# Performance work log

Measured on AMD Instinct MI355X. Metric: run time of the kernel, lower is better.

The kernel has to match this reference:

```python
import jax, jax.numpy as jnp
import numpy as np

N_NODES = 10000
N_EDGES = 160000
IN_FEATS = 512
H_FEATS = 512
NUM_CLASSES = 128


def setup_inputs() -> dict:
    key = jax.random.key(0)
    ks = jax.random.split(key, 7)
    h = jax.random.normal(ks[0], (N_NODES, IN_FEATS), dtype=jnp.float32)
    W1 = jax.random.normal(ks[1], (2 * IN_FEATS, H_FEATS), dtype=jnp.float32) * 0.02
    b1 = jax.random.normal(ks[2], (H_FEATS,), dtype=jnp.float32) * 0.02
    W2 = jax.random.normal(ks[3], (2 * H_FEATS, NUM_CLASSES), dtype=jnp.float32) * 0.02
    b2 = jax.random.normal(ks[4], (NUM_CLASSES,), dtype=jnp.float32) * 0.02
    src = jax.random.randint(ks[5], (N_EDGES,), 0, N_NODES, dtype=jnp.int32)
    dst = jax.random.randint(ks[6], (N_EDGES,), 0, N_NODES, dtype=jnp.int32)
    return {"h": h, "W1": W1, "b1": b1, "W2": W2, "b2": b2, "src": src, "dst": dst}


def _weighted_sage_conv(h, W, b, src, dst, n_nodes):
    # message = u_mul_e('h','w') with w == ones -> just gather source features
    msg = h[src]  # [E, d]
    # fn.mean reduce at destination: segment-sum / in-degree (0 if no in-edges)
    s = jax.ops.segment_sum(msg, dst, num_segments=n_nodes)  # [N, d]
    cnt = jax.ops.segment_sum(jnp.ones((src.shape[0],), h.dtype), dst, num_segments=n_nodes)
    h_N = s / jnp.maximum(cnt, 1.0)[:, None]
    h_total = jnp.concatenate([h, h_N], axis=1)  # [N, 2d]
    return h_total @ W + b


def reference(h, W1, b1, W2, b2, src, dst):
    n = h.shape[0]
    h1 = jax.nn.relu(_weighted_sage_conv(h, W1, b1, src, dst, n))
    return _weighted_sage_conv(h1, W2, b2, src, dst, n)
```

## Files before the change

### kernel.cpp

```cpp
#include <hip/hip_runtime.h>

typedef unsigned short u16;
typedef unsigned char u8;
typedef __attribute__((ext_vector_type(2))) float floatx2;
typedef __attribute__((ext_vector_type(4))) float floatx4;
typedef __attribute__((ext_vector_type(8))) __bf16 bf16x8;
typedef __attribute__((ext_vector_type(2))) unsigned short us2;
typedef __attribute__((ext_vector_type(4))) unsigned short us4;
typedef __attribute__((ext_vector_type(8))) unsigned short us8;
typedef __attribute__((ext_vector_type(2))) unsigned int u32x2;

static __device__ __forceinline__ float b2f(u16 v) {
    union { unsigned u; float f; } x; x.u = ((unsigned)v) << 16; return x.f;
}
static __device__ __forceinline__ u16 f2b(float f) {
    union { float f; unsigned u; } x; x.f = f;
    unsigned u = x.u;
    return (u16)((u + 0x7fffu + ((u >> 16) & 1u)) >> 16);
}

#define GLOAD_LDS16(g, l) __builtin_amdgcn_global_load_lds( \
    (const __attribute__((address_space(1))) void*)(g),     \
    (__attribute__((address_space(3))) void*)(l), 16, 0, 0)

#define CAP 64
#define SPILLMAX 4096

static __device__ __forceinline__ int detect_blk(const u16* __restrict__ p,
                                                 int nelem, int* sh) {
    if (threadIdx.x == 0) *sh = 0;
    __syncthreads();
    const int lim = nelem < 512 ? nelem : 512;
    int found = 0;
    for (int j = threadIdx.x; 2 * j < lim; j += 256) {
        unsigned v = p[2 * j] & 0x7fffu;
        if (v >= 0x4280u) found = 1;
    }
    if (found) atomicOr(sh, 1);
    __syncthreads();
    return *sh;
}

static __device__ __forceinline__ int xcd_swz(int L, int nwg) {
    const int q = nwg >> 3, r = nwg & 7;
    const int x = L & 7, i = L >> 3;
    return (x < r ? x * (q + 1) : r * (q + 1) + (x - r) * q) + i;
}

__global__ __launch_bounds__(256) void k_d1(
    const int* __restrict__ src, const int* __restrict__ dst, int E, int Nn,
    int* __restrict__ cnt, int* __restrict__ bucket,
    int* __restrict__ nspill, int* __restrict__ spill,
    const void* __restrict__ h, const void* __restrict__ W1,
    const void* __restrict__ b1, const void* __restrict__ W2,
    const void* __restrict__ b2,
    u16* __restrict__ Hb, u16* __restrict__ W1T, u16* __restrict__ W2T,
    u16* __restrict__ b1c, u16* __restrict__ b2c, int* __restrict__ flags,
    int nFill, int nHb) {
    __shared__ u16 tile[32][33];
    __shared__ int sh;
    const int b = blockIdx.x;
    const int t = threadIdx.x;

    if (b < nFill) {
        int e = b * 256 + t;
        if (e < E) {
            int d = dst[e], s = src[e];
            if ((unsigned)d < (unsigned)Nn && (unsigned)s < (unsigned)Nn) {
                int p = atomicAdd(&cnt[d], 1);
                if (p < CAP) bucket[d * CAP + p] = s;
                else {
                    int q = atomicAdd(nspill, 1);
                    if (q < SPILLMAX) { spill[2 * q] = d; spill[2 * q + 1] = s; }
                }
            }
        }
        return;
    }
    if (b < nFill + nHb) {
        const int f = detect_blk((const u16*)h, Nn * 512, &sh);
        int i = ((b - nFill) * 256 + t) * 8;
        if (i >= Nn * 512) return;
        if (f) {
            const floatx4* s = (const floatx4*)((const float*)h + i);
            floatx4 v0 = s[0], v1 = s[1];
            us8 o;
            o[0] = f2b(v0[0]); o[1] = f2b(v0[1]); o[2] = f2b(v0[2]); o[3] = f2b(v0[3]);
            o[4] = f2b(v1[0]); o[5] = f2b(v1[1]); o[6] = f2b(v1[2]); o[7] = f2b(v1[3]);
            *(us8*)(Hb + i) = o;
        } else {
            *(us8*)(Hb + i) = *(const us8*)((const u16*)h + i);
        }
        return;
    }
    if (b < nFill + nHb + 512) {
        const int f = detect_blk((const u16*)W1, 1024 * 512, &sh);
        int sub = b - nFill - nHb;
        int half = sub >> 8, idx = sub & 255;
        const int bx = (idx & 15) * 32, by = (idx >> 4) * 32;
        const int koff = half * 512, noff = half * 512;
        const int tx = t & 31, ty = t >> 5;
        for (int i = ty; i < 32; i += 8) {
            long id = (long)(koff + by + i) * 512 + (bx + tx);
            tile[i][tx] = f ? f2b(((const float*)W1)[id]) : ((const u16*)W1)[id];
        }
        __syncthreads();
        for (int i = ty; i < 32; i += 8)
            W1T[(long)(noff + bx + i) * 512 + (by + tx)] = tile[tx][i];
        return;
    }
    if (b < nFill + nHb + 640) {
        const int f = detect_blk((const u16*)W2, 1024 * 128, &sh);
        int sub = b - nFill - nHb - 512;
        int half = sub >> 6, idx = sub & 63;
        const int bx = (idx & 3) * 32, by = (idx >> 2) * 32;
        const int koff = half * 512, noff = half * 128;
        const int tx = t & 31, ty = t >> 5;
        for (int i = ty; i < 32; i += 8) {
            long id = (long)(koff + by + i) * 128 + (bx + tx);
            tile[i][tx] = f ? f2b(((const float*)W2)[id]) : ((const u16*)W2)[id];
        }
        __syncthreads();
        for (int i = ty; i < 32; i += 8)
            W2T[(long)(noff + bx + i) * 512 + (by + tx)] = tile[tx][i];
        return;
    }
    {
        const int f1 = detect_blk((const u16*)b1, 512, &sh);
        for (int i = t; i < 512; i += 256)
            b1c[i] = f1 ? f2b(((const float*)b1)[i]) : ((const u16*)b1)[i];
        const int f2 = detect_blk((const u16*)b2, 128, &sh);
        if (t < 128)
            b2c[t] = f2 ? f2b(((const float*)b2)[t]) : ((const u16*)b2)[t];
        const int fh = detect_blk((const u16*)h, Nn * 512, &sh);
        if (t == 0) flags[0] = fh;
    }
}

__device__ __forceinline__ void gemm_acc64(const u16* __restrict__ A,
                                           const u16* __restrict__ Bt,
                                           long brow, int bobs,
                                           floatx4 acc[4][2], u16* lA, u16* lB) {
    const int tid = threadIdx.x;
    const int wv = tid >> 6;
    const int ln = tid & 63;
    const int lrow = ln >> 2;
    const int lk = (ln & 3) * 8;
    const int m0 = ln & 15;
    const int kq = (ln >> 4) * 8;
    const int wc = wv * 32;

#pragma unroll
    for (int i = 0; i < 4; ++i)
#pragma unroll
        for (int j = 0; j < 2; ++j) acc[i][j] = (floatx4){0.f, 0.f, 0.f, 0.f};

    const u16* gA = A + (brow + wv * 16 + lrow) * 512 + lk;

    auto STAGE = [&](int kt, int sel) {
        u16* dA = lA + sel * 2048 + wv * 512;
        u16* dB = lB + sel * 4096;
        GLOAD_LDS16(gA + kt, dA);
#pragma unroll
        for (int ii = 0; ii < 2; ++ii) {
            const int c = ii * 4 + wv;
            GLOAD_LDS16(Bt + (long)(bobs + c * 16 + lrow) * 512 + kt + lk,
                        dB + c * 512);
        }
    };
    auto COMPUTE = [&](int sel) {
        const u16* rA = lA + sel * 2048;
        const u16* rB = lB + sel * 4096;
        bf16x8 af[4], bf[2];
#pragma unroll
        for (int i = 0; i < 4; ++i)
            af[i] = *(const bf16x8*)(rA + (i * 16 + m0) * 32 + kq);
#pragma unroll
        for (int j = 0; j < 2; ++j)
            bf[j] = *(const bf16x8*)(rB + (wc + j * 16 + m0) * 32 + kq);
#pragma unroll
        for (int i = 0; i < 4; ++i)
#pragma unroll
            for (int j = 0; j < 2; ++j)
                acc[i][j] = __builtin_amdgcn_mfma_f32_16x16x32_bf16(af[i], bf[j],
                                                                    acc[i][j], 0, 0, 0);
    };

    STAGE(0, 0);
    for (int t = 0; t < 15; ++t) {
        const int sel = t & 1;
        STAGE((t + 1) << 5, sel ^ 1);
        asm volatile("s_waitcnt vmcnt(3)" ::: "memory");
        __builtin_amdgcn_s_barrier();
        COMPUTE(sel);
        asm volatile("s_waitcnt lgkmcnt(0)" ::: "memory");
        __builtin_amdgcn_s_barrier();
    }
    asm volatile("s_waitcnt vmcnt(0)" ::: "memory");
    __builtin_amdgcn_s_barrier();
    COMPUTE(1);
}

__global__ __launch_bounds__(256) void k_gemm1_64(
    const u16* __restrict__ A, const u16* __restrict__ Bt,
    u16* __restrict__ C1s, u8* __restrict__ P1, int Mstore) {
    __shared__ __align__(16) u16 lA[2 * 64 * 32];
    __shared__ __align__(16) u16 lB[2 * 128 * 32];
    const int L = blockIdx.y * gridDim.x + blockIdx.x;
    const int T = xcd_swz(L, gridDim.x * gridDim.y);
    const int by = T & 7;
    const int bcol = by * 128;
    const long brow = (long)(T >> 3) * 64;
    floatx4 acc[4][2];
    gemm_acc64(A, Bt, brow, bcol, acc, lA, lB);

    const int ln = threadIdx.x & 63;
    const int wv = threadIdx.x >> 6;
    const int wc = wv * 32;
    const int m0 = ln & 15;
    const int q4 = (ln >> 4) * 4;
    if (by < 4) {
#pragma unroll
        for (int i = 0; i < 4; ++i)
#pragma unroll
            for (int r = 0; r < 4; ++r) {
                long row = brow + i * 16 + q4 + r;
                if (row < Mstore) {
#pragma unroll
                    for (int j = 0; j < 2; ++j)
                        C1s[row * 512 + (bcol + wc + j * 16 + m0)] = f2b(acc[i][j][r]);
                }
            }
    } else {
        const int coff = bcol - 512;
#pragma unroll
        for (int i = 0; i < 4; ++i)
#pragma unroll
            for (int r = 0; r < 4; ++r) {
                long row = brow + i * 16 + q4 + r;
                if (row < Mstore) {
#pragma unroll
                    for (int j = 0; j < 2; ++j) {
                        float v = acc[i][j][r];
                        int pk = __builtin_amdgcn_cvt_pk_fp8_f32(v, v, 0, false);
                        P1[row * 512 + (coff + wc + j * 16 + m0)] = (u8)(pk & 0xff);
                    }
                }
            }
    }
}

__global__ __launch_bounds__(256) void k_gemm2_64(
    const u16* __restrict__ A, const u16* __restrict__ Bt,
    u16* __restrict__ C2s, u16* __restrict__ P2, int Mstore) {
    __shared__ __align__(16) u16 lA[2 * 64 * 32];
    __shared__ __align__(16) u16 lB[2 * 128 * 32];
    const int L = blockIdx.y * gridDim.x + blockIdx.x;
    const int T = xcd_swz(L, gridDim.x * gridDim.y);
    const int by = T & 1;
    const long brow = (long)(T >> 1) * 64;
    floatx4 acc[4][2];
    gemm_acc64(A, Bt, brow, by * 128, acc, lA, lB);

    u16* C = by ? P2 : C2s;
    const int ln = threadIdx.x & 63;
    const int wv = threadIdx.x >> 6;
    const int wc = wv * 32;
    const int m0 = ln & 15;
    const int q4 = (ln >> 4) * 4;
#pragma unroll
    for (int i = 0; i < 4; ++i)
#pragma unroll
        for (int r = 0; r < 4; ++r) {
            long row = brow + i * 16 + q4 + r;
            if (row < Mstore) {
#pragma unroll
                for (int j = 0; j < 2; ++j)
                    C[row * 128 + (wc + j * 16 + m0)] = f2b(acc[i][j][r]);
            }
        }
}

__global__ __launch_bounds__(256) void agg_h1(const u8* __restrict__ P1,
                                              const u16* __restrict__ C1s,
                                              const u16* __restrict__ b1c,
                                              const int* __restrict__ cnt,
                                              const int* __restrict__ bucket,
                                              const int* __restrict__ nspill,
                                              const int* __restrict__ spill,
                                              u16* __restrict__ h1, int Nn) {
    const int n = blockIdx.x * 4 + (threadIdx.x >> 6);
    const int l = threadIdx.x & 63;
    if (n >= Nn) return;
    const int c = cnt[n];
    const int inb = c < CAP ? c : CAP;
    const int* bk = bucket + (long)n * CAP;
    float a0 = 0.f, a1 = 0.f, a2 = 0.f, a3 = 0.f;
    float a4 = 0.f, a5 = 0.f, a6 = 0.f, a7 = 0.f;
    int e = 0;
    for (; e + 7 < inb; e += 8) {
        u32x2 w[8];
#pragma unroll
        for (int q = 0; q < 8; ++q) {
            int s = bk[e + q];
            w[q] = *(const u32x2*)(P1 + (long)s * 512 + l * 8);
        }
#pragma unroll
        for (int q = 0; q < 8; ++q) {
            floatx2 f0 = __builtin_amdgcn_cvt_pk_f32_fp8(w[q][0], false);
            floatx2 f1 = __builtin_amdgcn_cvt_pk_f32_fp8(w[q][0], true);
            floatx2 f2 = __builtin_amdgcn_cvt_pk_f32_fp8(w[q][1], false);
            floatx2 f3 = __builtin_amdgcn_cvt_pk_f32_fp8(w[q][1], true);
            a0 += f0[0]; a1 += f0[1]; a2 += f1[0]; a3 += f1[1];
            a4 += f2[0]; a5 += f2[1]; a6 += f3[0]; a7 += f3[1];
        }
    }
    for (; e + 3 < inb; e += 4) {
        u32x2 w[4];
#pragma unroll
        for (int q = 0; q < 4; ++q) {
            int s = bk[e + q];
            w[q] = *(const u32x2*)(P1 + (long)s * 512 + l * 8);
        }
#pragma unroll
        for (int q = 0; q < 4; ++q) {
            floatx2 f0 = __builtin_amdgcn_cvt_pk_f32_fp8(w[q][0], false);
            floatx2 f1 = __builtin_amdgcn_cvt_pk_f32_fp8(w[q][0], true);
            floatx2 f2 = __builtin_amdgcn_cvt_pk_f32_fp8(w[q][1], false);
            floatx2 f3 = __builtin_amdgcn_cvt_pk_f32_fp8(w[q][1], true);
            a0 += f0[0]; a1 += f0[1]; a2 += f1[0]; a3 += f1[1];
            a4 += f2[0]; a5 += f2[1]; a6 += f3[0]; a7 += f3[1];
        }
    }
    for (; e < inb; ++e) {
        int s = bk[e];
        u32x2 w = *(const u32x2*)(P1 + (long)s * 512 + l * 8);
        floatx2 f0 = __builtin_amdgcn_cvt_pk_f32_fp8(w[0], false);
        floatx2 f1 = __builtin_amdgcn_cvt_pk_f32_fp8(w[0], true);
        floatx2 f2 = __builtin_amdgcn_cvt_pk_f32_fp8(w[1], false);
        floatx2 f3 = __builtin_amdgcn_cvt_pk_f32_fp8(w[1], true);
        a0 += f0[0]; a1 += f0[1]; a2 += f1[0]; a3 += f1[1];
        a4 += f2[0]; a5 += f2[1]; a6 += f3[0]; a7 += f3[1];
    }
    const int ns = *nspill;
    if (ns > 0) {
        int lim = ns < SPILLMAX ? ns : SPILLMAX;
        for (int q = 0; q < lim; ++q) {
            if (spill[2 * q] == n) {
                int s = spill[2 * q + 1];
                u32x2 w = *(const u32x2*)(P1 + (long)s * 512 + l * 8);
                floatx2 f0 = __builtin_amdgcn_cvt_pk_f32_fp8(w[0], false);
                floatx2 f1 = __builtin_amdgcn_cvt_pk_f32_fp8(w[0], true);
                floatx2 f2 = __builtin_amdgcn_cvt_pk_f32_fp8(w[1], false);
                floatx2 f3 = __builtin_amdgcn_cvt_pk_f32_fp8(w[1], true);
                a0 += f0[0]; a1 += f0[1]; a2 += f1[0]; a3 += f1[1];
                a4 += f2[0]; a5 += f2[1]; a6 += f3[0]; a7 += f3[1];
            }
        }
    }
    float inv = 1.0f / (float)(c > 1 ? c : 1);
    us8 sf = *(const us8*)(C1s + (long)n * 512 + l * 8);
    us8 bv = *(const us8*)(b1c + l * 8);
    us8 o;
    o[0] = f2b(fmaxf(b2f(sf[0]) + a0 * inv + b2f(bv[0]), 0.f));
    o[1] = f2b(fmaxf(b2f(sf[1]) + a1 * inv + b2f(bv[1]), 0.f));
    o[2] = f2b(fmaxf(b2f(sf[2]) + a2 * inv + b2f(bv[2]), 0.f));
    o[3] = f2b(fmaxf(b2f(sf[3]) + a3 * inv + b2f(bv[3]), 0.f));
    o[4] = f2b(fmaxf(b2f(sf[4]) + a4 * inv + b2f(bv[4]), 0.f));
    o[5] = f2b(fmaxf(b2f(sf[5]) + a5 * inv + b2f(bv[5]), 0.f));
    o[6] = f2b(fmaxf(b2f(sf[6]) + a6 * inv + b2f(bv[6]), 0.f));
    o[7] = f2b(fmaxf(b2f(sf[7]) + a7 * inv + b2f(bv[7]), 0.f));
    *(us8*)(h1 + (long)n * 512 + l * 8) = o;
}

__global__ __launch_bounds__(256) void agg_out(const u16* __restrict__ P2,
                                               const u16* __restrict__ C2s,
                                               const u16* __restrict__ b2c,
                                               const int* __restrict__ cnt,
                                               const int* __restrict__ bucket,
                                               const int* __restrict__ nspill,
                                               const int* __restrict__ spill,
                                               void* __restrict__ outv, int Nn,
                                               const int* __restrict__ flags) {
    const int n = blockIdx.x * 4 + (threadIdx.x >> 6);
    const int l = threadIdx.x & 63;
    if (n >= Nn) return;
    const int c = cnt[n];
    const int inb = c < CAP ? c : CAP;
    const int* bk = bucket + (long)n * CAP;
    float a0 = 0.f, a1 = 0.f;
    int e = 0;
    for (; e + 3 < inb; e += 4) {
        int s0 = bk[e], s1 = bk[e + 1], s2 = bk[e + 2], s3 = bk[e + 3];
        us2 v0 = *(const us2*)(P2 + (long)s0 * 128 + l * 2);
        us2 v1 = *(const us2*)(P2 + (long)s1 * 128 + l * 2);
        us2 v2 = *(const us2*)(P2 + (long)s2 * 128 + l * 2);
        us2 v3 = *(const us2*)(P2 + (long)s3 * 128 + l * 2);
        a0 += (b2f(v0[0]) + b2f(v1[0])) + (b2f(v2[0]) + b2f(v3[0]));
        a1 += (b2f(v0[1]) + b2f(v1[1])) + (b2f(v2[1]) + b2f(v3[1]));
    }
    for (; e < inb; ++e) {
        int s0 = bk[e];
        us2 v0 = *(const us2*)(P2 + (long)s0 * 128 + l * 2);
        a0 += b2f(v0[0]); a1 += b2f(v0[1]);
    }
    const int ns = *nspill;
    if (ns > 0) {
        int lim = ns < SPILLMAX ? ns : SPILLMAX;
        for (int q = 0; q < lim; ++q) {
            if (spill[2 * q] == n) {
                int s0 = spill[2 * q + 1];
                us2 v0 = *(const us2*)(P2 + (long)s0 * 128 + l * 2);
                a0 += b2f(v0[0]); a1 += b2f(v0[1]);
            }
        }
    }
    float inv = 1.0f / (float)(c > 1 ? c : 1);
    us2 sf = *(const us2*)(C2s + (long)n * 128 + l * 2);
    us2 bv = *(const us2*)(b2c + l * 2);
    float o0 = b2f(sf[0]) + a0 * inv + b2f(bv[0]);
    float o1 = b2f(sf[1]) + a1 * inv + b2f(bv[1]);
    if (flags[0]) {
        float* o = (float*)outv + (long)n * 128 + l * 2;
        o[0] = o0; o[1] = o1;
    } else {
        us2 ob; ob[0] = f2b(o0); ob[1] = f2b(o1);
        *(us2*)((u16*)outv + (long)n * 128 + l * 2) = ob;
    }
}

extern "C" void kernel_launch(void* const* d_in, const int* in_sizes, int n_in,
                              void* d_out, int out_size, void* d_ws, size_t ws_size,
                              hipStream_t stream) {
    const int D = 512, NCLS = 128;
    const int Nn = in_sizes[0] / D;
    const int E  = in_sizes[5];
    const int mtiles = (Nn + 127) / 128;
    const int mt64 = (Nn + 63) / 64;
    const int Mpad = mtiles * 128;
    const int nFill = (E + 255) / 256;
    const int nHb = (Nn * D / 8 + 255) / 256;

    const int* src = (const int*)d_in[5];
    const int* dst = (const int*)d_in[6];

    char* p = (char*)d_ws;
    u16* Hb  = (u16*)p; p += (size_t)Mpad * D * 2;
    u16* h1  = (u16*)p; p += (size_t)Mpad * D * 2;
    u16* C1s = (u16*)p; p += (size_t)Mpad * D * 2;
    u8*  P1  = (u8*)p;  p += (size_t)Mpad * D;
    u16* C2s = (u16*)p; p += (size_t)Mpad * NCLS * 2;
    u16* P2  = (u16*)p; p += (size_t)Mpad * NCLS * 2;
    u16* W1T = (u16*)p; p += (size_t)1024 * D * 2;
    u16* W2T = (u16*)p; p += (size_t)256 * D * 2;
    u16* b1c = (u16*)p; p += 1024;
    u16* b2c = (u16*)p; p += 1024;
    int* flags  = (int*)p; p += 256;
    int* cnt    = (int*)p; p += (size_t)(Nn + 60) * 4;
    int* nspill = cnt + Nn;
    int* bucket = (int*)p; p += (size_t)Nn * CAP * 4;
    int* spill  = (int*)p; p += (size_t)SPILLMAX * 2 * 4;

    hipMemsetAsync(cnt, 0, (size_t)(Nn + 60) * 4, stream);

    k_d1<<<nFill + nHb + 641, 256, 0, stream>>>(
        src, dst, E, Nn, cnt, bucket, nspill, spill,
        d_in[0], d_in[1], d_in[2], d_in[3], d_in[4],
        Hb, W1T, W2T, b1c, b2c, flags, nFill, nHb);

    k_gemm1_64<<<dim3(mt64, 8), 256, 0, stream>>>(Hb, W1T, C1s, P1, Nn);

    agg_h1<<<(Nn + 3) / 4, 256, 0, stream>>>(P1, C1s, b1c, cnt, bucket,
                                             nspill, spill, h1, Nn);

    k_gemm2_64<<<dim3(mt64, 2), 256, 0, stream>>>(h1, W2T, C2s, P2, Nn);

    agg_out<<<(Nn + 3) / 4, 256, 0, stream>>>(P2, C2s, b2c, cnt, bucket,
                                              nspill, spill, d_out, Nn, flags);
}
```

Measured before the change: 148.1 us.

## Fuse all stages into one persistent kernel with software grid barriers

Replaces the five separate kernel launches (preprocess, GEMM1, aggregate1, GEMM2, aggregate2) with one persistent kernel of 768 blocks. The blocks loop over virtual block indices and separate the stages with an atomic-counter grid barrier. This removes launch gaps and per-kernel tail effects between the dependent stages. The catch is that correctness depends on all 768 blocks being co-resident, and every stage now runs under a reduced occupancy bound and with grid-wide spin waits.

```diff
diff --git a/kernel.cpp b/kernel.cpp
--- a/kernel.cpp
+++ b/kernel.cpp
@@ -25,6 +25,7 @@
 
 #define CAP 64
 #define SPILLMAX 4096
+#define NBLK 768
 
 static __device__ __forceinline__ int detect_blk(const u16* __restrict__ p,
                                                  int nelem, int* sh) {
@@ -47,8 +48,26 @@
     return (x < r ? x * (q + 1) : r * (q + 1) + (x - r) * q) + i;
 }
 
-__global__ __launch_bounds__(256) void k_d1(
-    const int* __restrict__ src, const int* __restrict__ dst, int E, int Nn,
+static __device__ __forceinline__ void grid_sync(int* bar, int* gen) {
+    __syncthreads();
+    if (threadIdx.x == 0) {
+        __threadfence();
+        int g = atomicAdd(gen, 0);
+        int v = atomicAdd(bar, 1);
+        if (v == NBLK - 1) {
+            atomicExch(bar, 0);
+            __threadfence();
+            atomicAdd(gen, 1);
+        } else {
+            while (atomicAdd(gen, 0) == g) __builtin_amdgcn_s_sleep(2);
+        }
+        __threadfence();
+    }
+    __syncthreads();
+}
+
+static __device__ void d1_body(
+    int b, const int* __restrict__ src, const int* __restrict__ dst, int E, int Nn,
     int* __restrict__ cnt, int* __restrict__ bucket,
     int* __restrict__ nspill, int* __restrict__ spill,
     const void* __restrict__ h, const void* __restrict__ W1,
@@ -56,10 +75,8 @@
     const void* __restrict__ b2,
     u16* __restrict__ Hb, u16* __restrict__ W1T, u16* __restrict__ W2T,
     u16* __restrict__ b1c, u16* __restrict__ b2c, int* __restrict__ flags,
-    int nFill, int nHb) {
-    __shared__ u16 tile[32][33];
-    __shared__ int sh;
-    const int b = blockIdx.x;
+    int nFill, int nHb, u16* smem, int* shp) {
+    u16 (*tile)[33] = (u16(*)[33])smem;
     const int t = threadIdx.x;
 
     if (b < nFill) {
@@ -75,26 +92,23 @@
                 }
             }
         }
-        return;
-    }
-    if (b < nFill + nHb) {
-        const int f = detect_blk((const u16*)h, Nn * 512, &sh);
+    } else if (b < nFill + nHb) {
+        const int f = detect_blk((const u16*)h, Nn * 512, shp);
         int i = ((b - nFill) * 256 + t) * 8;
-        if (i >= Nn * 512) return;
-        if (f) {
-            const floatx4* s = (const floatx4*)((const float*)h + i);
-            floatx4 v0 = s[0], v1 = s[1];
-            us8 o;
-            o[0] = f2b(v0[0]); o[1] = f2b(v0[1]); o[2] = f2b(v0[2]); o[3] = f2b(v0[3]);
-            o[4] = f2b(v1[0]); o[5] = f2b(v1[1]); o[6] = f2b(v1[2]); o[7] = f2b(v1[3]);
-            *(us8*)(Hb + i) = o;
-        } else {
-            *(us8*)(Hb + i) = *(const us8*)((const u16*)h + i);
-        }
-        return;
-    }
-    if (b < nFill + nHb + 512) {
-        const int f = detect_blk((const u16*)W1, 1024 * 512, &sh);
+        if (i < Nn * 512) {
+            if (f) {
+                const floatx4* s = (const floatx4*)((const float*)h + i);
+                floatx4 v0 = s[0], v1 = s[1];
+                us8 o;
+                o[0] = f2b(v0[0]); o[1] = f2b(v0[1]); o[2] = f2b(v0[2]); o[3] = f2b(v0[3]);
+                o[4] = f2b(v1[0]); o[5] = f2b(v1[1]); o[6] = f2b(v1[2]); o[7] = f2b(v1[3]);
+                *(us8*)(Hb + i) = o;
+            } else {
+                *(us8*)(Hb + i) = *(const us8*)((const u16*)h + i);
+            }
+        }
+    } else if (b < nFill + nHb + 512) {
+        const int f = detect_blk((const u16*)W1, 1024 * 512, shp);
         int sub = b - nFill - nHb;
         int half = sub >> 8, idx = sub & 255;
         const int bx = (idx & 15) * 32, by = (idx >> 4) * 32;
@@ -107,10 +121,8 @@
         __syncthreads();
         for (int i = ty; i < 32; i += 8)
             W1T[(long)(noff + bx + i) * 512 + (by + tx)] = tile[tx][i];
-        return;
-    }
-    if (b < nFill + nHb + 640) {
-        const int f = detect_blk((const u16*)W2, 1024 * 128, &sh);
+    } else if (b < nFill + nHb + 640) {
+        const int f = detect_blk((const u16*)W2, 1024 * 128, shp);
         int sub = b - nFill - nHb - 512;
         int half = sub >> 6, idx = sub & 63;
         const int bx = (idx & 3) * 32, by = (idx >> 2) * 32;
@@ -123,16 +135,14 @@
         __syncthreads();
         for (int i = ty; i < 32; i += 8)
             W2T[(long)(noff + bx + i) * 512 + (by + tx)] = tile[tx][i];
-        return;
-    }
-    {
-        const int f1 = detect_blk((const u16*)b1, 512, &sh);
+    } else {
+        const int f1 = detect_blk((const u16*)b1, 512, shp);
         for (int i = t; i < 512; i += 256)
             b1c[i] = f1 ? f2b(((const float*)b1)[i]) : ((const u16*)b1)[i];
-        const int f2 = detect_blk((const u16*)b2, 128, &sh);
+        const int f2 = detect_blk((const u16*)b2, 128, shp);
         if (t < 128)
             b2c[t] = f2 ? f2b(((const float*)b2)[t]) : ((const u16*)b2)[t];
-        const int fh = detect_blk((const u16*)h, Nn * 512, &sh);
+        const int fh = detect_blk((const u16*)h, Nn * 512, shp);
         if (t == 0) flags[0] = fh;
     }
 }
@@ -201,97 +211,14 @@
     COMPUTE(1);
 }
 
-__global__ __launch_bounds__(256) void k_gemm1_64(
-    const u16* __restrict__ A, const u16* __restrict__ Bt,
-    u16* __restrict__ C1s, u8* __restrict__ P1, int Mstore) {
-    __shared__ __align__(16) u16 lA[2 * 64 * 32];
-    __shared__ __align__(16) u16 lB[2 * 128 * 32];
-    const int L = blockIdx.y * gridDim.x + blockIdx.x;
-    const int T = xcd_swz(L, gridDim.x * gridDim.y);
-    const int by = T & 7;
-    const int bcol = by * 128;
-    const long brow = (long)(T >> 3) * 64;
-    floatx4 acc[4][2];
-    gemm_acc64(A, Bt, brow, bcol, acc, lA, lB);
-
-    const int ln = threadIdx.x & 63;
-    const int wv = threadIdx.x >> 6;
-    const int wc = wv * 32;
-    const int m0 = ln & 15;
-    const int q4 = (ln >> 4) * 4;
-    if (by < 4) {
-#pragma unroll
-        for (int i = 0; i < 4; ++i)
-#pragma unroll
-            for (int r = 0; r < 4; ++r) {
-                long row = brow + i * 16 + q4 + r;
-                if (row < Mstore) {
-#pragma unroll
-                    for (int j = 0; j < 2; ++j)
-                        C1s[row * 512 + (bcol + wc + j * 16 + m0)] = f2b(acc[i][j][r]);
-                }
-            }
-    } else {
-        const int coff = bcol - 512;
-#pragma unroll
-        for (int i = 0; i < 4; ++i)
-#pragma unroll
-            for (int r = 0; r < 4; ++r) {
-                long row = brow + i * 16 + q4 + r;
-                if (row < Mstore) {
-#pragma unroll
-                    for (int j = 0; j < 2; ++j) {
-                        float v = acc[i][j][r];
-                        int pk = __builtin_amdgcn_cvt_pk_fp8_f32(v, v, 0, false);
-                        P1[row * 512 + (coff + wc + j * 16 + m0)] = (u8)(pk & 0xff);
-                    }
-                }
-            }
-    }
-}
-
-__global__ __launch_bounds__(256) void k_gemm2_64(
-    const u16* __restrict__ A, const u16* __restrict__ Bt,
-    u16* __restrict__ C2s, u16* __restrict__ P2, int Mstore) {
-    __shared__ __align__(16) u16 lA[2 * 64 * 32];
-    __shared__ __align__(16) u16 lB[2 * 128 * 32];
-    const int L = blockIdx.y * gridDim.x + blockIdx.x;
-    const int T = xcd_swz(L, gridDim.x * gridDim.y);
-    const int by = T & 1;
-    const long brow = (long)(T >> 1) * 64;
-    floatx4 acc[4][2];
-    gemm_acc64(A, Bt, brow, by * 128, acc, lA, lB);
-
-    u16* C = by ? P2 : C2s;
-    const int ln = threadIdx.x & 63;
-    const int wv = threadIdx.x >> 6;
-    const int wc = wv * 32;
-    const int m0 = ln & 15;
-    const int q4 = (ln >> 4) * 4;
-#pragma unroll
-    for (int i = 0; i < 4; ++i)
-#pragma unroll
-        for (int r = 0; r < 4; ++r) {
-            long row = brow + i * 16 + q4 + r;
-            if (row < Mstore) {
-#pragma unroll
-                for (int j = 0; j < 2; ++j)
-                    C[row * 128 + (wc + j * 16 + m0)] = f2b(acc[i][j][r]);
-            }
-        }
-}
-
-__global__ __launch_bounds__(256) void agg_h1(const u8* __restrict__ P1,
-                                              const u16* __restrict__ C1s,
-                                              const u16* __restrict__ b1c,
-                                              const int* __restrict__ cnt,
-                                              const int* __restrict__ bucket,
-                                              const int* __restrict__ nspill,
-                                              const int* __restrict__ spill,
-                                              u16* __restrict__ h1, int Nn) {
-    const int n = blockIdx.x * 4 + (threadIdx.x >> 6);
-    const int l = threadIdx.x & 63;
-    if (n >= Nn) return;
+static __device__ void agg_h1_body(int n, int l, const u8* __restrict__ P1,
+                                   const u16* __restrict__ C1s,
+                                   const u16* __restrict__ b1c,
+                                   const int* __restrict__ cnt,
+                                   const int* __restrict__ bucket,
+                                   const int* __restrict__ nspill,
+                                   const int* __restrict__ spill,
+                                   u16* __restrict__ h1) {
     const int c = cnt[n];
     const int inb = c < CAP ? c : CAP;
     const int* bk = bucket + (long)n * CAP;
@@ -373,18 +300,15 @@
     *(us8*)(h1 + (long)n * 512 + l * 8) = o;
 }
 
-__global__ __launch_bounds__(256) void agg_out(const u16* __restrict__ P2,
-                                               const u16* __restrict__ C2s,
-                                               const u16* __restrict__ b2c,
-                                               const int* __restrict__ cnt,
-                                               const int* __restrict__ bucket,
-                                               const int* __restrict__ nspill,
-                                               const int* __restrict__ spill,
-                                               void* __restrict__ outv, int Nn,
-                                               const int* __restrict__ flags) {
-    const int n = blockIdx.x * 4 + (threadIdx.x >> 6);
-    const int l = threadIdx.x & 63;
-    if (n >= Nn) return;
+static __device__ void agg_out_body(int n, int l, const u16* __restrict__ P2,
+                                    const u16* __restrict__ C2s,
+                                    const u16* __restrict__ b2c,
+                                    const int* __restrict__ cnt,
+                                    const int* __restrict__ bucket,
+                                    const int* __restrict__ nspill,
+                                    const int* __restrict__ spill,
+                                    void* __restrict__ outv,
+                                    const int* __restrict__ flags) {
     const int c = cnt[n];
     const int inb = c < CAP ? c : CAP;
     const int* bk = bucket + (long)n * CAP;
@@ -426,6 +350,121 @@
     } else {
         us2 ob; ob[0] = f2b(o0); ob[1] = f2b(o1);
         *(us2*)((u16*)outv + (long)n * 128 + l * 2) = ob;
+    }
+}
+
+__global__ __launch_bounds__(256, 4) void k_fused(
+    const int* __restrict__ src, const int* __restrict__ dst, int E, int Nn,
+    int* __restrict__ cnt, int* __restrict__ bucket,
+    int* __restrict__ nspill, int* __restrict__ spill,
+    const void* __restrict__ h, const void* __restrict__ W1,
+    const void* __restrict__ b1v, const void* __restrict__ W2,
+    const void* __restrict__ b2v,
+    u16* __restrict__ Hb, u16* __restrict__ W1T, u16* __restrict__ W2T,
+    u16* __restrict__ b1c, u16* __restrict__ b2c, int* __restrict__ flags,
+    u16* __restrict__ C1s, u8* __restrict__ P1, u16* __restrict__ h1,
+    u16* __restrict__ C2s, u16* __restrict__ P2, void* __restrict__ outv,
+    int* __restrict__ bar, int* __restrict__ gen,
+    int nFill, int nHb, int mt64) {
+    __shared__ __align__(16) u16 smem[12288];
+    __shared__ int sh;
+    u16* lA = smem;
+    u16* lB = smem + 4096;
+    const int tid = threadIdx.x;
+    const int ln = tid & 63;
+    const int wv = tid >> 6;
+
+    const int nA = nFill + nHb + 641;
+    for (int vb = blockIdx.x; vb < nA; vb += NBLK) {
+        __syncthreads();
+        d1_body(vb, src, dst, E, Nn, cnt, bucket, nspill, spill,
+                h, W1, b1v, W2, b2v, Hb, W1T, W2T, b1c, b2c, flags,
+                nFill, nHb, smem, &sh);
+    }
+    grid_sync(bar, gen);
+
+    const int nt1 = mt64 * 8;
+    for (int L = blockIdx.x; L < nt1; L += NBLK) {
+        __syncthreads();
+        const int T = xcd_swz(L, nt1);
+        const int by = T & 7;
+        const int bcol = by * 128;
+        const long brow = (long)(T >> 3) * 64;
+        floatx4 acc[4][2];
+        gemm_acc64(Hb, W1T, brow, bcol, acc, lA, lB);
+        const int wc = wv * 32;
+        const int m0 = ln & 15;
+        const int q4 = (ln >> 4) * 4;
+        if (by < 4) {
+#pragma unroll
+            for (int i = 0; i < 4; ++i)
+#pragma unroll
+                for (int r = 0; r < 4; ++r) {
+                    long row = brow + i * 16 + q4 + r;
+                    if (row < Nn) {
+#pragma unroll
+                        for (int j = 0; j < 2; ++j)
+                            C1s[row * 512 + (bcol + wc + j * 16 + m0)] =
+                                f2b(acc[i][j][r]);
+                    }
+                }
+        } else {
+            const int coff = bcol - 512;
+#pragma unroll
+            for (int i = 0; i < 4; ++i)
+#pragma unroll
+                for (int r = 0; r < 4; ++r) {
+                    long row = brow + i * 16 + q4 + r;
+                    if (row < Nn) {
+#pragma unroll
+                        for (int j = 0; j < 2; ++j) {
+                            float v = acc[i][j][r];
+                            int pk = __builtin_amdgcn_cvt_pk_fp8_f32(v, v, 0, false);
+                            P1[row * 512 + (coff + wc + j * 16 + m0)] = (u8)(pk & 0xff);
+                        }
+                    }
+                }
+        }
+    }
+    grid_sync(bar, gen);
+
+    const int nNd = (Nn + 3) >> 2;
+    for (int vb = blockIdx.x; vb < nNd; vb += NBLK) {
+        int n = vb * 4 + wv;
+        if (n < Nn) agg_h1_body(n, ln, P1, C1s, b1c, cnt, bucket, nspill, spill, h1);
+    }
+    grid_sync(bar, gen);
+
+    const int nt2 = mt64 * 2;
+    for (int L = blockIdx.x; L < nt2; L += NBLK) {
+        __syncthreads();
+        const int T = xcd_swz(L, nt2);
+        const int by2 = T & 1;
+        const long brow = (long)(T >> 1) * 64;
+        floatx4 acc[4][2];
+        gemm_acc64(h1, W2T, brow, by2 * 128, acc, lA, lB);
+        u16* C = by2 ? P2 : C2s;
+        const int wc = wv * 32;
+        const int m0 = ln & 15;
+        const int q4 = (ln >> 4) * 4;
+#pragma unroll
+        for (int i = 0; i < 4; ++i)
+#pragma unroll
+            for (int r = 0; r < 4; ++r) {
+                long row = brow + i * 16 + q4 + r;
+                if (row < Nn) {
+#pragma unroll
+                    for (int j = 0; j < 2; ++j)
+                        C[row * 128 + (wc + j * 16 + m0)] = f2b(acc[i][j][r]);
+                }
+            }
+    }
+    grid_sync(bar, gen);
+
+    for (int vb = blockIdx.x; vb < nNd; vb += NBLK) {
+        int n = vb * 4 + wv;
+        if (n < Nn) agg_out_body(n, ln, P2, C2s, b2c, cnt, bucket, nspill, spill,
+                                 outv, flags);
     }
 }
 
@@ -458,23 +497,17 @@
     int* flags  = (int*)p; p += 256;
     int* cnt    = (int*)p; p += (size_t)(Nn + 60) * 4;
     int* nspill = cnt + Nn;
+    int* bar    = cnt + Nn + 16;
+    int* gen    = cnt + Nn + 32;
     int* bucket = (int*)p; p += (size_t)Nn * CAP * 4;
     int* spill  = (int*)p; p += (size_t)SPILLMAX * 2 * 4;
 
     hipMemsetAsync(cnt, 0, (size_t)(Nn + 60) * 4, stream);
 
-    k_d1<<<nFill + nHb + 641, 256, 0, stream>>>(
+    k_fused<<<NBLK, 256, 0, stream>>>(
         src, dst, E, Nn, cnt, bucket, nspill, spill,
         d_in[0], d_in[1], d_in[2], d_in[3], d_in[4],
-        Hb, W1T, W2T, b1c, b2c, flags, nFill, nHb);
-
-    k_gemm1_64<<<dim3(mt64, 8), 256, 0, stream>>>(Hb, W1T, C1s, P1, Nn);
-
-    agg_h1<<<(Nn + 3) / 4, 256, 0, stream>>>(P1, C1s, b1c, cnt, bucket,
-                                             nspill, spill, h1, Nn);
-
-    k_gemm2_64<<<dim3(mt64, 2), 256, 0, stream>>>(h1, W2T, C2s, P2, Nn);
-
-    agg_out<<<(Nn + 3) / 4, 256, 0, stream>>>(P2, C2s, b2c, cnt, bucket,
-                                              nspill, spill, d_out, Nn, flags);
-}
+        Hb, W1T, W2T, b1c, b2c, flags,
+        C1s, P1, h1, C2s, P2, d_out,
+        bar, gen, nFill, nHb, mt64);
+}
```

After: 549.9 us. +271.4%, slower.

## Double GEMM K-tile to 64 with XOR-swizzled LDS layout

Applied to the files above, without the earlier changes.

Raises the shared GEMM routine's K step from 32 to 64, so the main loop runs half as many iterations with half as many barriers and more loads in flight per stage. The global-to-LDS copy now writes rows with an XOR swizzle on the 16-byte column index, and the fragment reads apply the same swizzle to avoid LDS bank conflicts. Each block's LDS use doubles to 48 KB, which may lower the number of blocks resident per CU.

```diff
diff --git a/kernel.cpp b/kernel.cpp
--- a/kernel.cpp
+++ b/kernel.cpp
@@ -144,10 +144,11 @@
     const int tid = threadIdx.x;
     const int wv = tid >> 6;
     const int ln = tid & 63;
-    const int lrow = ln >> 2;
-    const int lk = (ln & 3) * 8;
+    const int rlow = ln >> 3;
+    const int cpos = ln & 7;
+    const int csrc = (cpos ^ rlow) * 8;
     const int m0 = ln & 15;
-    const int kq = (ln >> 4) * 8;
+    const int g4 = ln >> 4;
     const int wc = wv * 32;
 
 #pragma unroll
@@ -155,42 +156,47 @@
 #pragma unroll
         for (int j = 0; j < 2; ++j) acc[i][j] = (floatx4){0.f, 0.f, 0.f, 0.f};
 
-    const u16* gA = A + (brow + wv * 16 + lrow) * 512 + lk;
-
     auto STAGE = [&](int kt, int sel) {
-        u16* dA = lA + sel * 2048 + wv * 512;
-        u16* dB = lB + sel * 4096;
-        GLOAD_LDS16(gA + kt, dA);
-#pragma unroll
-        for (int ii = 0; ii < 2; ++ii) {
-            const int c = ii * 4 + wv;
-            GLOAD_LDS16(Bt + (long)(bobs + c * 16 + lrow) * 512 + kt + lk,
-                        dB + c * 512);
+#pragma unroll
+        for (int q = 0; q < 2; ++q) {
+            const int r = wv * 16 + q * 8 + rlow;
+            GLOAD_LDS16(A + (brow + r) * 512 + kt + csrc,
+                        lA + sel * 4096 + wv * 1024 + q * 512);
+        }
+#pragma unroll
+        for (int q = 0; q < 4; ++q) {
+            const int r = wv * 32 + q * 8 + rlow;
+            GLOAD_LDS16(Bt + (long)(bobs + r) * 512 + kt + csrc,
+                        lB + sel * 8192 + wv * 2048 + q * 512);
         }
     };
     auto COMPUTE = [&](int sel) {
-        const u16* rA = lA + sel * 2048;
-        const u16* rB = lB + sel * 4096;
-        bf16x8 af[4], bf[2];
-#pragma unroll
-        for (int i = 0; i < 4; ++i)
-            af[i] = *(const bf16x8*)(rA + (i * 16 + m0) * 32 + kq);
-#pragma unroll
-        for (int j = 0; j < 2; ++j)
-            bf[j] = *(const bf16x8*)(rB + (wc + j * 16 + m0) * 32 + kq);
-#pragma unroll
-        for (int i = 0; i < 4; ++i)
+        const u16* rA = lA + sel * 4096;
+        const u16* rB = lB + sel * 8192;
+#pragma unroll
+        for (int kk = 0; kk < 2; ++kk) {
+            const int p = ((kk * 4 + g4) ^ (m0 & 7)) * 8;
+            bf16x8 af[4], bf[2];
+#pragma unroll
+            for (int i = 0; i < 4; ++i)
+                af[i] = *(const bf16x8*)(rA + (i * 16 + m0) * 64 + p);
 #pragma unroll
             for (int j = 0; j < 2; ++j)
-                acc[i][j] = __builtin_amdgcn_mfma_f32_16x16x32_bf16(af[i], bf[j],
-                                                                    acc[i][j], 0, 0, 0);
+                bf[j] = *(const bf16x8*)(rB + (wc + j * 16 + m0) * 64 + p);
+#pragma unroll
+            for (int i = 0; i < 4; ++i)
+#pragma unroll
+                for (int j = 0; j < 2; ++j)
+                    acc[i][j] = __builtin_amdgcn_mfma_f32_16x16x32_bf16(
+                        af[i], bf[j], acc[i][j], 0, 0, 0);
+        }
     };
 
     STAGE(0, 0);
-    for (int t = 0; t < 15; ++t) {
+    for (int t = 0; t < 7; ++t) {
         const int sel = t & 1;
-        STAGE((t + 1) << 5, sel ^ 1);
-        asm volatile("s_waitcnt vmcnt(3)" ::: "memory");
+        STAGE((t + 1) << 6, sel ^ 1);
+        asm volatile("s_waitcnt vmcnt(6)" ::: "memory");
         __builtin_amdgcn_s_barrier();
         COMPUTE(sel);
         asm volatile("s_waitcnt lgkmcnt(0)" ::: "memory");
@@ -204,8 +210,8 @@
 __global__ __launch_bounds__(256) void k_gemm1_64(
     const u16* __restrict__ A, const u16* __restrict__ Bt,
     u16* __restrict__ C1s, u8* __restrict__ P1, int Mstore) {
-    __shared__ __align__(16) u16 lA[2 * 64 * 32];
-    __shared__ __align__(16) u16 lB[2 * 128 * 32];
+    __shared__ __align__(16) u16 lA[2 * 64 * 64];
+    __shared__ __align__(16) u16 lB[2 * 128 * 64];
     const int L = blockIdx.y * gridDim.x + blockIdx.x;
     const int T = xcd_swz(L, gridDim.x * gridDim.y);
     const int by = T & 7;
@@ -253,8 +259,8 @@
 __global__ __launch_bounds__(256) void k_gemm2_64(
     const u16* __restrict__ A, const u16* __restrict__ Bt,
     u16* __restrict__ C2s, u16* __restrict__ P2, int Mstore) {
-    __shared__ __align__(16) u16 lA[2 * 64 * 32];
-    __shared__ __align__(16) u16 lB[2 * 128 * 32];
+    __shared__ __align__(16) u16 lA[2 * 64 * 64];
+    __shared__ __align__(16) u16 lB[2 * 128 * 64];
     const int L = blockIdx.y * gridDim.x + blockIdx.x;
     const int T = xcd_swz(L, gridDim.x * gridDim.y);
     const int by = T & 1;
```

Result: faster. 143.6 us (median of 2 runs) (-3.0%).
